# Optimization experiments

Measured on AMD Instinct MI355X. Metric: run time of the kernel, lower is better.

## Reference

```python
import jax, jax.numpy as jnp
import numpy as np
import math

V, D, H, FF, L, S, B = 32000, 1024, 16, 4096, 8, 1024, 4
HD = D // H


def _pos_encoding(seq_len, dim):
    pos = np.arange(seq_len)[:, None].astype(np.float32)
    div = np.exp(np.arange(0, dim, 2).astype(np.float32) * -(math.log(10000.0) / dim))
    pe = np.zeros((seq_len, dim), dtype=np.float32)
    pe[:, 0::2] = np.sin(pos * div)
    pe[:, 1::2] = np.cos(pos * div)
    return jnp.asarray(pe)


def setup_inputs() -> dict:
    key = jax.random.key(0)
    ks = jax.random.split(key, 24)
    sc = 0.02
    inp = {
        'tokens': jax.random.randint(ks[0], (B, S), 0, V),
        'emb_W': jax.random.normal(ks[1], (V, D), jnp.float32) * sc,
        'Wq': jax.random.normal(ks[2], (L, D, D), jnp.float32) * sc,
        'bq': jnp.zeros((L, D), jnp.float32),
        'Wk': jax.random.normal(ks[3], (L, D, D), jnp.float32) * sc,
        'bk': jnp.zeros((L, D), jnp.float32),
        'Wv': jax.random.normal(ks[4], (L, D, D), jnp.float32) * sc,
        'bv': jnp.zeros((L, D), jnp.float32),
        'Wo': jax.random.normal(ks[5], (L, D, D), jnp.float32) * sc,
        'bo': jnp.zeros((L, D), jnp.float32),
        'ln1_g': jnp.ones((L, D), jnp.float32),
        'ln1_b': jnp.zeros((L, D), jnp.float32),
        'ln2_g': jnp.ones((L, D), jnp.float32),
        'ln2_b': jnp.zeros((L, D), jnp.float32),
        'W1': jax.random.normal(ks[6], (L, D, FF), jnp.float32) * sc,
        'b1': jnp.zeros((L, FF), jnp.float32),
        'W2': jax.random.normal(ks[7], (L, FF, D), jnp.float32) * sc,
        'b2': jnp.zeros((L, D), jnp.float32),
        'lnf_g': jnp.ones((D,), jnp.float32),
        'lnf_b': jnp.zeros((D,), jnp.float32),
        'head_W': jax.random.normal(ks[8], (D, V), jnp.float32) * sc,
        'head_b': jnp.zeros((V,), jnp.float32),
    }
    return inp


def _layernorm(x, g, b, eps=1e-5):
    mu = jnp.mean(x, axis=-1, keepdims=True)
    var = jnp.mean(jnp.square(x - mu), axis=-1, keepdims=True)
    return (x - mu) * jax.lax.rsqrt(var + eps) * g + b


def _attention(x, Wq, bq, Wk, bk, Wv, bv, Wo, bo, causal_mask):
    b, s, d = x.shape
    q = (x @ Wq + bq).reshape(b, s, H, HD).transpose(0, 2, 1, 3)
    k = (x @ Wk + bk).reshape(b, s, H, HD).transpose(0, 2, 1, 3)
    v = (x @ Wv + bv).reshape(b, s, H, HD).transpose(0, 2, 1, 3)
    scores = jnp.einsum('bhqd,bhkd->bhqk', q, k) / math.sqrt(HD)
    scores = jnp.where(causal_mask, scores, -1e9)
    attn = jax.nn.softmax(scores, axis=-1)
    out = jnp.einsum('bhqk,bhkd->bhqd', attn, v)
    out = out.transpose(0, 2, 1, 3).reshape(b, s, d)
    return out @ Wo + bo


def reference(tokens, emb_W, Wq, bq, Wk, bk, Wv, bv, Wo, bo,
              ln1_g, ln1_b, ln2_g, ln2_b, W1, b1, W2, b2,
              lnf_g, lnf_b, head_W, head_b):
    b, s = tokens.shape
    mask = jnp.tril(jnp.ones((s, s), bool))[None, None]  # (1,1,s,s)
    x = emb_W[tokens] + _pos_encoding(s, D)[None]
    for l in range(L):
        a = _attention(_layernorm(x, ln1_g[l], ln1_b[l]),
                       Wq[l], bq[l], Wk[l], bk[l], Wv[l], bv[l], Wo[l], bo[l], mask)
        x = x + a
        h = _layernorm(x, ln2_g[l], ln2_b[l])
        h = jax.nn.relu(h @ W1[l] + b1[l]) @ W2[l] + b2[l]
        x = x + h
    x = _layernorm(x, lnf_g, lnf_b)
    return x @ head_W + head_b
```

## Files before the change

### kernel.cpp

```cpp
#include <hip/hip_runtime.h>
#include <math.h>


using u16 = unsigned short;
using u32 = unsigned int;
typedef __attribute__((ext_vector_type(4))) float  f32x4;
typedef __attribute__((ext_vector_type(8))) short  s16x8;
typedef __attribute__((ext_vector_type(8))) __bf16 bf16x8;

__device__ __forceinline__ u16 f2bf(float f) {
  u32 u = __builtin_bit_cast(u32, f);
  u += 0x7fffu + ((u >> 16) & 1u);
  return (u16)(u >> 16);
}

__device__ __forceinline__ f32x4 mfma16(s16x8 a, s16x8 b, f32x4 c) {
  return __builtin_amdgcn_mfma_f32_16x16x32_bf16(
      __builtin_bit_cast(bf16x8, a), __builtin_bit_cast(bf16x8, b), c, 0, 0, 0);
}

#define GLD16(gp, lp) __builtin_amdgcn_global_load_lds(                    \
    (const __attribute__((address_space(1))) void*)(gp),                   \
    (__attribute__((address_space(3))) void*)(lp), 16, 0, 0)

__global__ __launch_bounds__(256) void transpose_cvt(
    const float* __restrict__ in, u16* __restrict__ out,
    int C, long long inLS, long long outLS, int outRS)
{
  __shared__ float t[32][33];
  int tr = threadIdx.x >> 5, tc = threadIdx.x & 31;
  const float* ip = in + (size_t)blockIdx.z * inLS +
                    ((size_t)blockIdx.x * 32 + tr) * C + blockIdx.y * 32 + tc;
#pragma unroll
  for (int p = 0; p < 4; ++p) t[p * 8 + tr][tc] = ip[(size_t)p * 8 * C];
  __syncthreads();
  u16* op = out + (size_t)blockIdx.z * outLS +
            ((size_t)blockIdx.y * 32 + tr) * outRS + (size_t)blockIdx.x * 32 + tc;
#pragma unroll
  for (int p = 0; p < 4; ++p) op[(size_t)p * 8 * outRS] = f2bf(t[tc][p * 8 + tr]);
}

__global__ __launch_bounds__(256) void pack_bqkv(
    const float* __restrict__ bq, const float* __restrict__ bk,
    const float* __restrict__ bv, float* __restrict__ outb)
{
  int i = blockIdx.x * 256 + threadIdx.x;
  int ly = i / 3072, j = i % 3072;
  float v = (j < 1024) ? bq[ly * 1024 + j]
          : (j < 2048) ? bk[ly * 1024 + (j - 1024)]
                       : bv[ly * 1024 + (j - 2048)];
  outb[i] = v;
}

__global__ __launch_bounds__(256) void embed_kernel(
    const int* __restrict__ tokens, const float* __restrict__ embW,
    float* __restrict__ x)
{
  int row = blockIdx.x;
  int s = row & 1023;
  int tok = tokens[row];
  int d0 = threadIdx.x * 4;
  float4 e = *(const float4*)&embW[(size_t)tok * 1024 + d0];
  const float c = -9.210340371976184f / 1024.0f;
  float div0 = expf((float)d0 * c);
  float div1 = expf((float)(d0 + 2) * c);
  float sn0, cs0, sn1, cs1;
  sincosf((float)s * div0, &sn0, &cs0);
  sincosf((float)s * div1, &sn1, &cs1);
  float4 r;
  r.x = e.x + sn0; r.y = e.y + cs0; r.z = e.z + sn1; r.w = e.w + cs1;
  *(float4*)&x[(size_t)row * 1024 + d0] = r;
}

__global__ __launch_bounds__(256) void ln_kernel(
    const float* __restrict__ x, const float* __restrict__ g,
    const float* __restrict__ b, u16* __restrict__ y)
{
  int row = blockIdx.x, tid = threadIdx.x;
  float4 v = *(const float4*)&x[(size_t)row * 1024 + tid * 4];
  float sum = v.x + v.y + v.z + v.w;
  float sq = v.x * v.x + v.y * v.y + v.z * v.z + v.w * v.w;
#pragma unroll
  for (int o = 32; o > 0; o >>= 1) {
    sum += __shfl_xor(sum, o, 64);
    sq  += __shfl_xor(sq,  o, 64);
  }
  __shared__ float ps[8];
  int w = tid >> 6;
  if ((tid & 63) == 0) { ps[w] = sum; ps[4 + w] = sq; }
  __syncthreads();
  sum = ps[0] + ps[1] + ps[2] + ps[3];
  sq  = ps[4] + ps[5] + ps[6] + ps[7];
  float mu = sum * (1.0f / 1024.0f);
  float var = sq * (1.0f / 1024.0f) - mu * mu;
  float rs = rsqrtf(var + 1e-5f);
  float4 gg = *(const float4*)&g[tid * 4];
  float4 bb = *(const float4*)&b[tid * 4];
  u32 lo = (u32)f2bf((v.x - mu) * rs * gg.x + bb.x) |
           ((u32)f2bf((v.y - mu) * rs * gg.y + bb.y) << 16);
  u32 hi = (u32)f2bf((v.z - mu) * rs * gg.z + bb.z) |
           ((u32)f2bf((v.w - mu) * rs * gg.w + bb.w) << 16);
  uint2 o2; o2.x = lo; o2.y = hi;
  *(uint2*)&y[(size_t)row * 1024 + tid * 4] = o2;
}

__global__ __launch_bounds__(256) void ff2_reduce(
    const float* __restrict__ p, const float* __restrict__ b2,
    float* __restrict__ x)
{
  int row = blockIdx.x, c = threadIdx.x * 4;
  size_t idx = (size_t)row * 1024 + c;
  f32x4 v  = *(f32x4*)&x[idx];
  f32x4 a0 = *(const f32x4*)&p[idx];
  f32x4 a1 = *(const f32x4*)&p[idx + 4194304];
  f32x4 a2 = *(const f32x4*)&p[idx + 8388608];
  f32x4 a3 = *(const f32x4*)&p[idx + 12582912];
  f32x4 bb = *(const f32x4*)&b2[c];
  v = v + a0 + a1 + a2 + a3 + bb;
  *(f32x4*)&x[idx] = v;
}

template<int OMODE, int RELU, int MAP>
__global__ __launch_bounds__(512, 2) void gemm256(
    const u16* __restrict__ A, int lda, const u16* __restrict__ Bt,
    const float* __restrict__ bias, void* Cp, int M, int N, int klen,
    int gxp8, int gxreal)
{
  __shared__ alignas(16) u16 lds[2][32768];
  const int tid = threadIdx.x;
  const int w = tid >> 6, l = tid & 63;
  const int g = l >> 4, lr = l & 15;
  const int wm = w >> 2, wn = w & 3;
  const int bid = blockIdx.x;
  const int xcd = bid & 7, k = bid >> 3;
  int by, bx, split = 0;
  if (MAP == 0) {
    int t = k >> 5, j = k & 31;
    int s = xcd + 8 * t;
    by = (s / gxp8) * 4 + (j & 3);
    bx = (s % gxp8) * 8 + (j >> 2);
    if (bx >= gxreal) return;
  } else {
    split = bid & 3;
    by = (bid >> 2) & 15;
    bx = bid >> 6;
  }
  const int m0 = by << 8, n0 = bx << 8;
  const u16* Ab = A  + (split << 10);
  const u16* Bb = Bt + (split << 10);

  const u16* Ag[4]; const u16* Bg[4]; int dstE[4];
#pragma unroll
  for (int s2 = 0; s2 < 4; ++s2) {
    int idx = s2 * 512 + tid;
    int row = idx >> 3;
    int ch = (idx & 7) ^ (row & 7);
    Ag[s2] = Ab + (size_t)(m0 + row) * lda + ch * 8;
    Bg[s2] = Bb + (size_t)(n0 + row) * lda + ch * 8;
    dstE[s2] = idx * 8;
  }
  const int colx0 = ((g)     ^ (lr & 7)) * 8;
  const int colx1 = ((4 + g) ^ (lr & 7)) * 8;
  const int abase = (wm * 128 + lr) * 64;
  const int bbase = 16384 + (wn * 64 + lr) * 64;

  f32x4 acc[8][4];
#pragma unroll
  for (int i = 0; i < 8; ++i)
#pragma unroll
    for (int j2 = 0; j2 < 4; ++j2) acc[i][j2] = f32x4{0.f, 0.f, 0.f, 0.f};

  const int nk = klen >> 6;
#pragma unroll
  for (int s2 = 0; s2 < 4; ++s2) GLD16(Ag[s2], &lds[0][dstE[s2]]);
#pragma unroll
  for (int s2 = 0; s2 < 4; ++s2) GLD16(Bg[s2], &lds[0][16384 + dstE[s2]]);
  asm volatile("s_waitcnt vmcnt(0)" ::: "memory");
  __builtin_amdgcn_s_barrier();

  int cur = 0;
  for (int t = 0; t < nk; ++t) {
    const bool more = (t + 1 < nk);
    if (more) {
      const int kn = (t + 1) << 6;
#pragma unroll
      for (int s2 = 0; s2 < 4; ++s2) GLD16(Ag[s2] + kn, &lds[cur ^ 1][dstE[s2]]);
#pragma unroll
      for (int s2 = 0; s2 < 4; ++s2) GLD16(Bg[s2] + kn, &lds[cur ^ 1][16384 + dstE[s2]]);
    }
    s16x8 a0[8], b0[4], a1[8], b1[4];
#pragma unroll
    for (int mf = 0; mf < 8; ++mf) a0[mf] = *(const s16x8*)&lds[cur][abase + mf * 1024 + colx0];
#pragma unroll
    for (int nf = 0; nf < 4; ++nf) b0[nf] = *(const s16x8*)&lds[cur][bbase + nf * 1024 + colx0];
#pragma unroll
    for (int mf = 0; mf < 8; ++mf) a1[mf] = *(const s16x8*)&lds[cur][abase + mf * 1024 + colx1];
#pragma unroll
    for (int nf = 0; nf < 4; ++nf) b1[nf] = *(const s16x8*)&lds[cur][bbase + nf * 1024 + colx1];
    __builtin_amdgcn_s_setprio(1);
#pragma unroll
    for (int mf = 0; mf < 8; ++mf)
#pragma unroll
      for (int nf = 0; nf < 4; ++nf) acc[mf][nf] = mfma16(a0[mf], b0[nf], acc[mf][nf]);
#pragma unroll
    for (int mf = 0; mf < 8; ++mf)
#pragma unroll
      for (int nf = 0; nf < 4; ++nf) acc[mf][nf] = mfma16(a1[mf], b1[nf], acc[mf][nf]);
    __builtin_amdgcn_s_setprio(0);
    if (more) {
      asm volatile("s_waitcnt vmcnt(0)" ::: "memory");
      __builtin_amdgcn_s_barrier();
      cur ^= 1;
    }
  }

  float* fst = (float*)(void*)&lds[0][0];
  float* Cf = (OMODE == 3)
            ? ((float*)Cp + (size_t)split * ((size_t)M * N))
            : (float*)Cp;
#pragma unroll
  for (int mf = 0; mf < 8; ++mf) {
    __builtin_amdgcn_s_barrier();
#pragma unroll
    for (int nf = 0; nf < 4; ++nf) {
      int cl = wn * 64 + nf * 16 + lr;
      float bv = 0.f;
      if (OMODE != 3) bv = bias[n0 + cl];
      int rl = wm * 16 + g * 4;
#pragma unroll
      for (int r = 0; r < 4; ++r) {
        float v = acc[mf][nf][r] + bv;
        if (RELU) v = fmaxf(v, 0.f);
        fst[(rl + r) * 260 + cl] = v;
      }
    }
    __builtin_amdgcn_s_barrier();
    if (OMODE == 0) {
#pragma unroll
      for (int it = 0; it < 2; ++it) {
        int seg = it * 512 + tid;
        int row = seg >> 5;
        int co  = (seg & 31) * 8;
        int grow = m0 + (row >> 4) * 128 + mf * 16 + (row & 15);
        const float* src = &fst[row * 260 + co];
        uint4 q;
        q.x = (u32)f2bf(src[0]) | ((u32)f2bf(src[1]) << 16);
        q.y = (u32)f2bf(src[2]) | ((u32)f2bf(src[3]) << 16);
        q.z = (u32)f2bf(src[4]) | ((u32)f2bf(src[5]) << 16);
        q.w = (u32)f2bf(src[6]) | ((u32)f2bf(src[7]) << 16);
        *(uint4*)&((u16*)Cp)[(size_t)grow * N + n0 + co] = q;
      }
    } else {
#pragma unroll
      for (int it = 0; it < 4; ++it) {
        int seg = it * 512 + tid;
        int row = seg >> 6;
        int co  = (seg & 63) * 4;
        int grow = m0 + (row >> 4) * 128 + mf * 16 + (row & 15);
        f32x4 q = *(const f32x4*)&fst[row * 260 + co];
        *(f32x4*)&Cf[(size_t)grow * N + n0 + co] = q;
      }
    }
  }
}

template<int OMODE, int RELU>
__global__ __launch_bounds__(256, 3) void gemm_p(
    const u16* __restrict__ A, const u16* __restrict__ Bt,
    const float* __restrict__ bias, const float* res, void* Cp,
    int M, int N, int K, int gx)
{
  __shared__ alignas(16) u16 lds[2][8192];
  const int tid = threadIdx.x;
  const int w = tid >> 6, l = tid & 63;
  const int g = l >> 4, lr = l & 15;
  const int wm = w >> 1, wn = w & 1;
  int nwg = gridDim.x;
  int bid = blockIdx.x;
  int swz = (bid & 7) * (nwg >> 3) + (bid >> 3);
  int bx = swz % gx, by = swz / gx;
  int m0 = by << 7, n0 = bx << 7;

  const u16 *Ag[2], *Bg[2];
  int dstA[2], dstB[2];
#pragma unroll
  for (int s = 0; s < 2; ++s) {
    int idx = s * 256 + tid;
    int row = idx >> 2;
    int ch = (idx & 3) ^ ((row >> 1) & 3);
    Ag[s] = A  + (size_t)(m0 + row) * K + ch * 8;
    Bg[s] = Bt + (size_t)(n0 + row) * K + ch * 8;
    dstA[s] = idx * 8;
    dstB[s] = 4096 + idx * 8;
  }
  const int colx = (g ^ ((lr >> 1) & 3)) * 8;
  const int aoff = (wm * 64 + lr) * 32 + colx;
  const int boff = 4096 + (wn * 64 + lr) * 32 + colx;

  f32x4 acc[4][4];
#pragma unroll
  for (int i = 0; i < 4; ++i)
#pragma unroll
    for (int j = 0; j < 4; ++j) acc[i][j] = f32x4{0.f, 0.f, 0.f, 0.f};

  const int nk = K >> 5;
#pragma unroll
  for (int s = 0; s < 2; ++s) GLD16(Ag[s], &lds[0][dstA[s]]);
#pragma unroll
  for (int s = 0; s < 2; ++s) GLD16(Bg[s], &lds[0][dstB[s]]);
  asm volatile("s_waitcnt vmcnt(0)" ::: "memory");
  __builtin_amdgcn_s_barrier();

  int cur = 0;
  s16x8 aC[4], bC[4];
#pragma unroll
  for (int i = 0; i < 4; ++i) aC[i] = *(const s16x8*)&lds[0][aoff + i * 512];
#pragma unroll
  for (int j = 0; j < 4; ++j) bC[j] = *(const s16x8*)&lds[0][boff + j * 512];

  for (int t = 0; t < nk; ++t) {
    const bool more = (t + 1 < nk);
    if (more) {
      const int kn = (t + 1) << 5;
#pragma unroll
      for (int s = 0; s < 2; ++s) GLD16(Ag[s] + kn, &lds[cur ^ 1][dstA[s]]);
#pragma unroll
      for (int s = 0; s < 2; ++s) GLD16(Bg[s] + kn, &lds[cur ^ 1][dstB[s]]);
    }
    __builtin_amdgcn_s_setprio(1);
#pragma unroll
    for (int i = 0; i < 4; ++i)
#pragma unroll
      for (int j = 0; j < 4; ++j) acc[i][j] = mfma16(aC[i], bC[j], acc[i][j]);
    __builtin_amdgcn_s_setprio(0);
    if (more) {
      asm volatile("s_waitcnt vmcnt(0)" ::: "memory");
      __builtin_amdgcn_s_barrier();
      cur ^= 1;
#pragma unroll
      for (int i = 0; i < 4; ++i) aC[i] = *(const s16x8*)&lds[cur][aoff + i * 512];
#pragma unroll
      for (int j = 0; j < 4; ++j) bC[j] = *(const s16x8*)&lds[cur][boff + j * 512];
    }
  }
#pragma unroll
  for (int mf = 0; mf < 4; ++mf) {
    int row = m0 + wm * 64 + mf * 16 + g * 4;
#pragma unroll
    for (int nf = 0; nf < 4; ++nf) {
      int col = n0 + wn * 64 + nf * 16 + lr;
      float bv = bias[col];
#pragma unroll
      for (int r = 0; r < 4; ++r) {
        float v = acc[mf][nf][r] + bv;
        if (RELU) v = fmaxf(v, 0.f);
        size_t idx = (size_t)(row + r) * N + col;
        if (OMODE == 0)      ((u16*)Cp)[idx] = f2bf(v);
        else if (OMODE == 1) ((float*)Cp)[idx] = v + res[idx];
        else                 ((float*)Cp)[idx] = v;
      }
    }
  }
}

__global__ __launch_bounds__(256) void attn_kernel(
    const u16* __restrict__ qkv, u16* __restrict__ outp)
{
  int b = blockIdx.x >> 4, h = blockIdx.x & 15;
  int q0 = blockIdx.y << 6;
  int tid = threadIdx.x, w = tid >> 6, l = tid & 63;
  int g = l >> 4, lr = l & 15;
  const int RS = 3072;
  const u16* base = qkv + (size_t)b * 1024 * RS + h * 64;
  const u16* Qb = base;
  const u16* Kb = base + 1024;
  const u16* Vb = base + 2048;
  __shared__ alignas(16) u16 Plds[4][1024];
  __shared__ alignas(16) u16 Vt[4096];
  char* Pw = (char*)&Plds[w][0];

  s16x8 qf[2];
#pragma unroll
  for (int ks = 0; ks < 2; ++ks)
    qf[ks] = *(const s16x8*)&Qb[(size_t)(q0 + w * 16 + lr) * RS + ks * 32 + g * 8];

  f32x4 o[4];
#pragma unroll
  for (int n = 0; n < 4; ++n) o[n] = f32x4{0.f, 0.f, 0.f, 0.f};
  float mr[4] = {-INFINITY, -INFINITY, -INFINITY, -INFINITY};
  float ls[4] = {0.f, 0.f, 0.f, 0.f};

  int ntile = (q0 >> 6) + 1;
  for (int kt = 0; kt < ntile; ++kt) {
    int kv0 = kt << 6;
    f32x4 sc[4];
#pragma unroll
    for (int t = 0; t < 4; ++t) sc[t] = f32x4{0.f, 0.f, 0.f, 0.f};
#pragma unroll
    for (int ks = 0; ks < 2; ++ks)
#pragma unroll
      for (int t = 0; t < 4; ++t) {
        s16x8 kf = *(const s16x8*)&Kb[(size_t)(kv0 + t * 16 + lr) * RS + ks * 32 + g * 8];
        sc[t] = mfma16(qf[ks], kf, sc[t]);
      }
#pragma unroll
    for (int p = 0; p < 2; ++p) {
      int key = p * 32 + (tid >> 3);
      int d0 = (tid & 7) * 8;
      s16x8 vrow = *(const s16x8*)&Vb[(size_t)(kv0 + key) * RS + d0];
#pragma unroll
      for (int j = 0; j < 8; ++j) {
        int d = d0 + j;
        int byt = (d * 128 + key * 2) ^ ((d & 7) << 4);
        *(u16*)((char*)Vt + byt) = (u16)vrow[j];
      }
    }
    float p4[4][4];
    float tmax[4] = {-INFINITY, -INFINITY, -INFINITY, -INFINITY};
    int qr_base = q0 + w * 16 + g * 4;
#pragma unroll
    for (int t = 0; t < 4; ++t) {
      int key = kv0 + t * 16 + lr;
#pragma unroll
      for (int r = 0; r < 4; ++r) {
        float s = sc[t][r] * 0.125f;
        s = (key <= qr_base + r) ? s : -1e30f;
        p4[t][r] = s;
        tmax[r] = fmaxf(tmax[r], s);
      }
    }
#pragma unroll
    for (int off = 1; off < 16; off <<= 1)
#pragma unroll
      for (int r = 0; r < 4; ++r) tmax[r] = fmaxf(tmax[r], __shfl_xor(tmax[r], off, 64));
    float corr[4], rsum[4];
#pragma unroll
    for (int r = 0; r < 4; ++r) {
      float mn = fmaxf(mr[r], tmax[r]);
      corr[r] = __expf(mr[r] - mn);
      mr[r] = mn;
      rsum[r] = 0.f;
    }
#pragma unroll
    for (int t = 0; t < 4; ++t)
#pragma unroll
      for (int r = 0; r < 4; ++r) {
        float e = __expf(p4[t][r] - mr[r]);
        p4[t][r] = e;
        rsum[r] += e;
      }
#pragma unroll
    for (int off = 1; off < 16; off <<= 1)
#pragma unroll
      for (int r = 0; r < 4; ++r) rsum[r] += __shfl_xor(rsum[r], off, 64);
#pragma unroll
    for (int r = 0; r < 4; ++r) ls[r] = ls[r] * corr[r] + rsum[r];
#pragma unroll
    for (int n = 0; n < 4; ++n)
#pragma unroll
      for (int r = 0; r < 4; ++r) o[n][r] *= corr[r];
#pragma unroll
    for (int t = 0; t < 4; ++t)
#pragma unroll
      for (int r = 0; r < 4; ++r) {
        int prow = g * 4 + r;
        int byt = (prow * 128 + (t * 16 + lr) * 2) ^ ((prow & 7) << 4);
        *(u16*)(Pw + byt) = f2bf(p4[t][r]);
      }
    __syncthreads();
#pragma unroll
    for (int ks = 0; ks < 2; ++ks) {
      int ab = (lr * 128 + ks * 64 + g * 16) ^ ((lr & 7) << 4);
      s16x8 pa = *(const s16x8*)(Pw + ab);
#pragma unroll
      for (int n = 0; n < 4; ++n) {
        int vb2 = ((n * 16 + lr) * 128 + ks * 64 + g * 16) ^ ((lr & 7) << 4);
        s16x8 vfr = *(const s16x8*)((const char*)Vt + vb2);
        o[n] = mfma16(pa, vfr, o[n]);
      }
    }
    __syncthreads();
  }
#pragma unroll
  for (int n = 0; n < 4; ++n)
#pragma unroll
    for (int r = 0; r < 4; ++r) {
      float v = o[n][r] / ls[r];
      outp[(size_t)(b * 1024 + q0 + w * 16 + g * 4 + r) * 1024 + h * 64 + n * 16 + lr] = f2bf(v);
    }
}

extern "C" void kernel_launch(void* const* d_in, const int* in_sizes, int n_in,
                              void* d_out, int out_size, void* d_ws, size_t ws_size,
                              hipStream_t stream)
{
  const int*   tokens = (const int*)  d_in[0];
  const float* embW   = (const float*)d_in[1];
  const float* Wq     = (const float*)d_in[2];
  const float* bq     = (const float*)d_in[3];
  const float* Wk     = (const float*)d_in[4];
  const float* bk     = (const float*)d_in[5];
  const float* Wv     = (const float*)d_in[6];
  const float* bv     = (const float*)d_in[7];
  const float* Wo     = (const float*)d_in[8];
  const float* bo     = (const float*)d_in[9];
  const float* ln1g   = (const float*)d_in[10];
  const float* ln1b   = (const float*)d_in[11];
  const float* ln2g   = (const float*)d_in[12];
  const float* ln2b   = (const float*)d_in[13];
  const float* W1     = (const float*)d_in[14];
  const float* b1     = (const float*)d_in[15];
  const float* W2     = (const float*)d_in[16];
  const float* b2     = (const float*)d_in[17];
  const float* lnfg   = (const float*)d_in[18];
  const float* lnfb   = (const float*)d_in[19];
  const float* headW  = (const float*)d_in[20];
  const float* headb  = (const float*)d_in[21];
  (void)in_sizes; (void)n_in; (void)out_size;

  char* ws = (char*)d_ws;
  u16*   qkvT = (u16*)(ws);
  u16*   woT  = (u16*)(ws + 50331648);
  u16*   w1T  = (u16*)(ws + 67108864);
  u16*   w2T  = (u16*)(ws + 134217728);
  u16*   headT= (u16*)(ws + 201326592);
  float* bqkv = (float*)(ws + 266862592);
  float* x    = (float*)(ws + 266960896);
  u16*   y    = (u16*)(ws + 283738112);
  u16*   qkv  = (u16*)(ws + 292126720);
  u16*   attno= (u16*)(ws + 317292544);
  u16*   h1   = (u16*)(ws + 325681152);
  float* pbuf = (float*)(ws + 359235584);
  if (ws_size < 359235584ull) return;
  const bool splitk = (ws_size >= 426344448ull);

  dim3 blk(256);
  dim3 blk5(512);
  transpose_cvt<<<dim3(32, 32, 8),  blk, 0, stream>>>(Wq, qkvT,           1024,  1048576LL, 3145728LL, 1024);
  transpose_cvt<<<dim3(32, 32, 8),  blk, 0, stream>>>(Wk, qkvT + 1048576, 1024,  1048576LL, 3145728LL, 1024);
  transpose_cvt<<<dim3(32, 32, 8),  blk, 0, stream>>>(Wv, qkvT + 2097152, 1024,  1048576LL, 3145728LL, 1024);
  transpose_cvt<<<dim3(32, 32, 8),  blk, 0, stream>>>(Wo, woT,            1024,  1048576LL, 1048576LL, 1024);
  transpose_cvt<<<dim3(32, 128, 8), blk, 0, stream>>>(W1, w1T,            4096,  4194304LL, 4194304LL, 1024);
  transpose_cvt<<<dim3(128, 32, 8), blk, 0, stream>>>(W2, w2T,            1024,  4194304LL, 4194304LL, 4096);
  transpose_cvt<<<dim3(32, 1000, 1),blk, 0, stream>>>(headW, headT,       32000, 0LL,       0LL,       1024);
  pack_bqkv<<<96, blk, 0, stream>>>(bq, bk, bv, bqkv);
  embed_kernel<<<4096, blk, 0, stream>>>(tokens, embW, x);
  for (int ly = 0; ly < 8; ++ly) {
    ln_kernel<<<4096, blk, 0, stream>>>(x, ln1g + ly * 1024, ln1b + ly * 1024, y);
    gemm256<0, 0, 0><<<256, blk5, 0, stream>>>(y, 1024,
        qkvT + (size_t)ly * 3145728, bqkv + ly * 3072, qkv,
        4096, 3072, 1024, 2, 12);
    attn_kernel<<<dim3(64, 16), blk, 0, stream>>>(qkv, attno);
    gemm_p<1, 0><<<256, blk, 0, stream>>>(attno, woT + (size_t)ly * 1048576,
        bo + ly * 1024, x, x, 4096, 1024, 1024, 8);
    ln_kernel<<<4096, blk, 0, stream>>>(x, ln2g + ly * 1024, ln2b + ly * 1024, y);
    gemm256<0, 1, 0><<<256, blk5, 0, stream>>>(y, 1024,
        w1T + (size_t)ly * 4194304, b1 + ly * 4096, h1,
        4096, 4096, 1024, 2, 16);
    if (splitk) {
      gemm256<3, 0, 1><<<256, blk5, 0, stream>>>(h1, 4096,
          w2T + (size_t)ly * 4194304, nullptr, pbuf,
          4096, 1024, 1024, 0, 0);
      ff2_reduce<<<4096, blk, 0, stream>>>(pbuf, b2 + ly * 1024, x);
    } else {
      gemm_p<1, 0><<<256, blk, 0, stream>>>(h1, w2T + (size_t)ly * 4194304,
          b2 + ly * 1024, x, x, 4096, 1024, 4096, 8);
    }
  }
  ln_kernel<<<4096, blk, 0, stream>>>(x, lnfg, lnfb, y);
  gemm256<2, 0, 0><<<2048, blk5, 0, stream>>>(y, 1024, headT, headb,
      (float*)d_out, 4096, 32000, 1024, 16, 125);
}
```

Baseline: 2.349 ms.

## Switch GEMM main loop to 4-stage K=32 LDS pipeline with register prefetch

The 256x256 bf16 GEMM mainloop moves from a double-buffered K=64 scheme to a four-buffer ring of K=32 slices, keeping up to three global-to-LDS loads in flight. Waits use partial vmcnt counts instead of draining all loads each step. The next slice's fragments are read into registers while the second half of the current MFMAs runs, which is meant to hide global-load and LDS latency. In exchange each step does half the K work, so it pays for two barriers per step, and the new swizzle and wait counts add risk.

Result: slower. 2.454 ms (+4.5%).

```diff
diff --git a/kernel.cpp b/kernel.cpp
--- a/kernel.cpp
+++ b/kernel.cpp
@@ -126,7 +126,7 @@
     const float* __restrict__ bias, void* Cp, int M, int N, int klen,
     int gxp8, int gxreal)
 {
-  __shared__ alignas(16) u16 lds[2][32768];
+  __shared__ alignas(16) u16 lds[4][16384];
   const int tid = threadIdx.x;
   const int w = tid >> 6, l = tid & 63;
   const int g = l >> 4, lr = l & 15;
@@ -149,20 +149,19 @@
   const u16* Ab = A  + (split << 10);
   const u16* Bb = Bt + (split << 10);
 
-  const u16* Ag[4]; const u16* Bg[4]; int dstE[4];
-#pragma unroll
-  for (int s2 = 0; s2 < 4; ++s2) {
+  const u16* Ag[2]; const u16* Bg[2]; int dstE[2];
+#pragma unroll
+  for (int s2 = 0; s2 < 2; ++s2) {
     int idx = s2 * 512 + tid;
-    int row = idx >> 3;
-    int ch = (idx & 7) ^ (row & 7);
+    int row = idx >> 2;
+    int ch = (idx & 3) ^ ((row >> 1) & 3);
     Ag[s2] = Ab + (size_t)(m0 + row) * lda + ch * 8;
     Bg[s2] = Bb + (size_t)(n0 + row) * lda + ch * 8;
     dstE[s2] = idx * 8;
   }
-  const int colx0 = ((g)     ^ (lr & 7)) * 8;
-  const int colx1 = ((4 + g) ^ (lr & 7)) * 8;
-  const int abase = (wm * 128 + lr) * 64;
-  const int bbase = 16384 + (wn * 64 + lr) * 64;
+  const int colx = (g ^ ((lr >> 1) & 3)) * 8;
+  const int aoff = (wm * 128 + lr) * 32 + colx;
+  const int boff = 8192 + (wn * 64 + lr) * 32 + colx;
 
   f32x4 acc[8][4];
 #pragma unroll
@@ -170,48 +169,68 @@
 #pragma unroll
     for (int j2 = 0; j2 < 4; ++j2) acc[i][j2] = f32x4{0.f, 0.f, 0.f, 0.f};
 
-  const int nk = klen >> 6;
-#pragma unroll
-  for (int s2 = 0; s2 < 4; ++s2) GLD16(Ag[s2], &lds[0][dstE[s2]]);
-#pragma unroll
-  for (int s2 = 0; s2 < 4; ++s2) GLD16(Bg[s2], &lds[0][16384 + dstE[s2]]);
-  asm volatile("s_waitcnt vmcnt(0)" ::: "memory");
+  const int nk = klen >> 5;
+#pragma unroll
+  for (int pt = 0; pt < 3; ++pt) {
+    u16* buf = &lds[pt][0];
+#pragma unroll
+    for (int s2 = 0; s2 < 2; ++s2) GLD16(Ag[s2] + pt * 32, buf + dstE[s2]);
+#pragma unroll
+    for (int s2 = 0; s2 < 2; ++s2) GLD16(Bg[s2] + pt * 32, buf + 8192 + dstE[s2]);
+  }
+  asm volatile("s_waitcnt vmcnt(8)" ::: "memory");
   __builtin_amdgcn_s_barrier();
 
-  int cur = 0;
+  u16* p0 = &lds[0][0];
+  u16* p1 = &lds[1][0];
+  u16* p2 = &lds[2][0];
+  u16* p3 = &lds[3][0];
+
+  s16x8 aC[4], bC[4];
+#pragma unroll
+  for (int i = 0; i < 4; ++i) aC[i] = *(const s16x8*)&p0[aoff + i * 512];
+#pragma unroll
+  for (int j2 = 0; j2 < 4; ++j2) bC[j2] = *(const s16x8*)&p0[boff + j2 * 512];
+
   for (int t = 0; t < nk; ++t) {
-    const bool more = (t + 1 < nk);
-    if (more) {
-      const int kn = (t + 1) << 6;
-#pragma unroll
-      for (int s2 = 0; s2 < 4; ++s2) GLD16(Ag[s2] + kn, &lds[cur ^ 1][dstE[s2]]);
-#pragma unroll
-      for (int s2 = 0; s2 < 4; ++s2) GLD16(Bg[s2] + kn, &lds[cur ^ 1][16384 + dstE[s2]]);
-    }
-    s16x8 a0[8], b0[4], a1[8], b1[4];
-#pragma unroll
-    for (int mf = 0; mf < 8; ++mf) a0[mf] = *(const s16x8*)&lds[cur][abase + mf * 1024 + colx0];
-#pragma unroll
-    for (int nf = 0; nf < 4; ++nf) b0[nf] = *(const s16x8*)&lds[cur][bbase + nf * 1024 + colx0];
-#pragma unroll
-    for (int mf = 0; mf < 8; ++mf) a1[mf] = *(const s16x8*)&lds[cur][abase + mf * 1024 + colx1];
-#pragma unroll
-    for (int nf = 0; nf < 4; ++nf) b1[nf] = *(const s16x8*)&lds[cur][bbase + nf * 1024 + colx1];
+    const int rem = nk - 1 - t;
+    s16x8 aH[4];
+#pragma unroll
+    for (int i = 0; i < 4; ++i) aH[i] = *(const s16x8*)&p0[aoff + (4 + i) * 512];
+    if (rem >= 3) {
+      const int k3 = t * 32 + 96;
+#pragma unroll
+      for (int s2 = 0; s2 < 2; ++s2) GLD16(Ag[s2] + k3, p3 + dstE[s2]);
+#pragma unroll
+      for (int s2 = 0; s2 < 2; ++s2) GLD16(Bg[s2] + k3, p3 + 8192 + dstE[s2]);
+    }
     __builtin_amdgcn_s_setprio(1);
 #pragma unroll
-    for (int mf = 0; mf < 8; ++mf)
-#pragma unroll
-      for (int nf = 0; nf < 4; ++nf) acc[mf][nf] = mfma16(a0[mf], b0[nf], acc[mf][nf]);
-#pragma unroll
-    for (int mf = 0; mf < 8; ++mf)
-#pragma unroll
-      for (int nf = 0; nf < 4; ++nf) acc[mf][nf] = mfma16(a1[mf], b1[nf], acc[mf][nf]);
+    for (int i = 0; i < 4; ++i)
+#pragma unroll
+      for (int j2 = 0; j2 < 4; ++j2) acc[i][j2] = mfma16(aC[i], bC[j2], acc[i][j2]);
     __builtin_amdgcn_s_setprio(0);
-    if (more) {
-      asm volatile("s_waitcnt vmcnt(0)" ::: "memory");
-      __builtin_amdgcn_s_barrier();
-      cur ^= 1;
-    }
+    if (rem >= 3)      asm volatile("s_waitcnt vmcnt(8)" ::: "memory");
+    else if (rem == 2) asm volatile("s_waitcnt vmcnt(4)" ::: "memory");
+    else if (rem == 1) asm volatile("s_waitcnt vmcnt(0)" ::: "memory");
+    __builtin_amdgcn_s_barrier();
+    s16x8 aN[4], bN[4];
+    if (rem >= 1) {
+#pragma unroll
+      for (int i = 0; i < 4; ++i) aN[i] = *(const s16x8*)&p1[aoff + i * 512];
+#pragma unroll
+      for (int j2 = 0; j2 < 4; ++j2) bN[j2] = *(const s16x8*)&p1[boff + j2 * 512];
+    }
+    __builtin_amdgcn_s_setprio(1);
+#pragma unroll
+    for (int i = 0; i < 4; ++i)
+#pragma unroll
+      for (int j2 = 0; j2 < 4; ++j2) acc[4 + i][j2] = mfma16(aH[i], bC[j2], acc[4 + i][j2]);
+    __builtin_amdgcn_s_setprio(0);
+    __builtin_amdgcn_s_barrier();
+    u16* tmp = p0; p0 = p1; p1 = p2; p2 = p3; p3 = tmp;
+#pragma unroll
+    for (int i = 0; i < 4; ++i) { aC[i] = aN[i]; bC[i] = bN[i]; }
   }
 
   float* fst = (float*)(void*)&lds[0][0];
```
